# Kernel tuning notes

Hardware: AMD Instinct MI355X
Metric: run time of the kernel (lower is better)

## Reference

```python
import jax, jax.numpy as jnp
import numpy as np

C_IN = 4
C_OUT = 8
K = 5            # kernel_size (hardcoded by reshape(25,2) in original)
N_ROT = 8
R_B = 8          # rot_basis_size
STRIDE = 1
PAD = 2
TWO_PI = 2.0 * np.pi
ROT_SCALE = TWO_PI / R_B


def B2(x):
    # quadratic B-spline, exactly as in the torch source
    return (-3 * (-0.5 + x) ** 2 * jnp.sign(0.5 - x)
            + (-1.5 + x) ** 2 * jnp.sign(1.5 - x)
            - 3 * (1 + 2 * x) ** 2 * jnp.sign(0.5 + x) / 4
            + (3 + 2 * x) ** 2 * jnp.sign(1.5 + x) / 4) / 4


def angle_dist(th1, th2):
    return jnp.mod(th2 - th1 + np.pi, TWO_PI) - np.pi


def make_kernel_stack(weights):
    # weights: (C_IN, R_B*K*K, C_OUT). M = K*K*R_B combined (spatial-center, rot-center) index;
    # original repeats each spatial center R_B times (np.repeat) and tiles rot centers K*K times.
    lidx = -(K // 2)
    coords = jnp.arange(lidx, K // 2 + 1, dtype=jnp.float32)
    grid = jnp.stack(jnp.meshgrid(coords, coords, indexing='ij'), axis=-1)  # (K,K,2), grid[i,j]=[i+l, j+l]
    centers_xy = jnp.repeat(grid.reshape(K * K, 2), R_B, axis=0)            # (M,2)
    rot_centers = jnp.tile(jnp.arange(R_B, dtype=jnp.float32) * ROT_SCALE, K * K)  # (M,)
    rot_sample = jnp.arange(N_ROT, dtype=jnp.float32) * (TWO_PI / N_ROT)    # (N_ROT,)

    def one_kernel(theta):
        c, s = jnp.cos(theta), jnp.sin(theta)
        x, y = grid[..., 0], grid[..., 1]
        xxs = jnp.stack([x * c - y * s, x * s + y * c], axis=-1)            # (K,K,2) rotated sample grid
        xx_diffs = centers_xy[None, None, :, :] - xxs[:, :, None, :]        # (K,K,M,2)
        xx_vals = jnp.prod(B2(xx_diffs), axis=-1)                           # (K,K,M) separable spatial spline
        rots = rot_sample + theta                                           # (N_ROT,)
        rot_vals = B2(angle_dist(rots[:, None], rot_centers[None, :]) / ROT_SCALE)  # (N_ROT,M)
        vals = xx_vals[:, :, None, :] * rot_vals[None, None, :, :]          # (K,K,N_ROT,M)
        # contract basis index m against weights -> (C_OUT, C_IN, N_ROT, K, K)
        return jnp.einsum('xyrm,imo->oirxy', vals, weights)

    ks = jax.vmap(one_kernel)(-rot_sample)  # (N_ROT, C_OUT, C_IN, N_ROT, K, K), matches torch.cat over -theta
    return ks.reshape(N_ROT * C_OUT, C_IN * N_ROT, K, K)


def setup_inputs() -> dict:
    key = jax.random.key(0)
    kx, kw = jax.random.split(key)
    X = jax.random.normal(kx, (8, C_IN, N_ROT, 256, 256), dtype=jnp.float32)
    weights = jax.random.normal(kw, (C_IN, R_B * K * K, C_OUT), dtype=jnp.float32)
    return {'X': X, 'weights': weights}


def reference(X, weights):
    ks = make_kernel_stack(weights)                       # (N_ROT*C_OUT, C_IN*N_ROT, K, K)
    B, c, d, H, W = X.shape
    Xr = X.reshape(B, c * d, H, W)
    out = jax.lax.conv_general_dilated(
        Xr, ks, window_strides=(STRIDE, STRIDE),
        padding=[(PAD, PAD), (PAD, PAD)],
        dimension_numbers=('NCHW', 'OIHW', 'NCHW'))        # (B, N_ROT*C_OUT, h, w)
    Bn, _, h, w = out.shape
    out = out.reshape(Bn, N_ROT, C_OUT, h, w).transpose(0, 2, 1, 3, 4)  # (B, C_OUT, N_ROT, h, w)
    return (TWO_PI / N_ROT) * out
```

## Files before the change

kernel.cpp:

```cpp
#include <hip/hip_runtime.h>
#include <hip/hip_fp16.h>
#include <math.h>

#define PI_F      3.14159265358979323846f
#define TWO_PI_F  6.28318530717958647692f
#define PI4_F     0.78539816339744830962f

typedef _Float16 f16x8 __attribute__((ext_vector_type(8)));
typedef float    f32x4 __attribute__((ext_vector_type(4)));

#define XH_OFF     ((size_t)1 << 20)
#define XH_BYTES   ((size_t)8 * 256 * 256 * 32 * 2)

__device__ __forceinline__ float sgn(float t) {
    return (t > 0.f) ? 1.f : ((t < 0.f) ? -1.f : 0.f);
}

__device__ __forceinline__ float b2(float x) {
    float a = x - 0.5f;
    float b = x - 1.5f;
    float c = 1.f + 2.f * x;
    float d = 3.f + 2.f * x;
    return (-3.f * a * a * sgn(0.5f - x)
            + b * b * sgn(1.5f - x)
            - 0.75f * c * c * sgn(0.5f + x)
            + 0.25f * d * d * sgn(1.5f + x)) * 0.25f;
}

__global__ void build_ks_kernel(const float* __restrict__ w, __half* __restrict__ ksh) {
    int g = blockIdx.x * 256 + threadIdx.x;
    if (g >= 64 * 32 * 25) return;
    int O = g & 63;
    int rest = g >> 6;
    int t = rest % 25;
    int I = rest / 25;
    int r0 = O >> 3, o = O & 7;
    int i = I >> 3, r = I & 7;
    int x = t / 5, y = t % 5;

    float theta = -(float)r0 * PI4_F;
    float cth = cosf(theta), sth = sinf(theta);
    float fx = (float)(x - 2), fy = (float)(y - 2);
    float xc = fx * cth - fy * sth;
    float yc = fx * sth + fy * cth;

    float rotv[8];
    float rs = (float)r * PI4_F + theta;
    #pragma unroll
    for (int mr = 0; mr < 8; ++mr) {
        float v = (float)mr * PI4_F - rs + PI_F;
        float md = fmodf(v, TWO_PI_F);
        if (md < 0.f) md += TWO_PI_F;
        rotv[mr] = b2((md - PI_F) / PI4_F);
    }

    float sum = 0.f;
    for (int mx = 0; mx < 25; ++mx) {
        float cx = (float)(mx / 5 - 2);
        float cy = (float)(mx % 5 - 2);
        float bx = b2(cx - xc) * b2(cy - yc);
        if (bx != 0.f) {
            const float* wp = w + (size_t)(i * 200 + mx * 8) * 8 + o;
            #pragma unroll
            for (int mr = 0; mr < 8; ++mr)
                sum = fmaf(bx * rotv[mr], wp[mr * 8], sum);
        }
    }
    ksh[(size_t)(t * 64 + O) * 32 + I] = __float2half(sum);
}

__global__ __launch_bounds__(256, 4) void hwc_kernel(const float* __restrict__ X,
                                                     __half* __restrict__ Xh) {
    int b = blockIdx.x >> 8;
    int h = blockIdx.x & 255;
    int ww = threadIdx.x;
    const float* Xb = X + ((size_t)b * 32) * 65536 + h * 256 + ww;

    union { __half hh[8]; uint4 u; } pk[4];
    #pragma unroll
    for (int c = 0; c < 32; ++c)
        pk[c >> 3].hh[c & 7] = __float2half(Xb[(size_t)c * 65536]);

    uint4* dst = (uint4*)(Xh + ((size_t)(b * 65536 + h * 256 + ww)) * 32);
    #pragma unroll
    for (int kk = 0; kk < 4; ++kk) dst[kk] = pk[kk].u;
}

__global__ __launch_bounds__(512, 2) void conv_hwc_kernel(const __half* __restrict__ Xh,
                                                          const __half* __restrict__ ksh,
                                                          float* __restrict__ out) {
    __shared__ uint4 xt[4 * 1297];

    int bid = blockIdx.x;
    int b   = bid >> 6;
    int rem = bid & 63;
    int h0  = (rem >> 3) << 5;
    int w0  = (rem & 7) << 5;
    int tid = threadIdx.x;

    const char* Xb = (const char*)Xh + (size_t)b * ((size_t)65536 * 64);

    for (int p = tid; p < 1296; p += 512) {
        int r = p / 36, c = p - (p / 36) * 36;
        int gh = h0 + r - 2;
        int gw = w0 + c - 2;
        uint4 v0 = make_uint4(0u, 0u, 0u, 0u), v1 = v0, v2 = v0, v3 = v0;
        if ((unsigned)gh < 256u && (unsigned)gw < 256u) {
            const uint4* s = (const uint4*)(Xb + ((size_t)(gh * 256 + gw)) * 64);
            v0 = s[0]; v1 = s[1]; v2 = s[2]; v3 = s[3];
        }
        xt[0 * 1297 + p] = v0;
        xt[1 * 1297 + p] = v1;
        xt[2 * 1297 + p] = v2;
        xt[3 * 1297 + p] = v3;
    }
    __syncthreads();

    int wave = tid >> 6, lane = tid & 63;
    int lO = lane & 15, ks4 = lane >> 4;
    int bidx = lO * 4 + ks4;
    const uint4* ksq = (const uint4*)ksh;

    f32x4 acc[8][4] = {};
    int baseA[8];
    #pragma unroll
    for (int m = 0; m < 8; ++m)
        baseA[m] = 1297 * ks4 + (wave * 4 + (m >> 1)) * 36 + (m & 1) * 16 + lO;

    f16x8 Bf[2][4];
    #pragma unroll
    for (int n = 0; n < 4; ++n)
        Bf[0][n] = __builtin_bit_cast(f16x8, ksq[n * 64 + bidx]);

    #pragma unroll
    for (int t = 0; t < 25; ++t) {
        const int cur = t & 1, nxt = cur ^ 1;

        if (t < 24) {
            const int t1 = t + 1;
            #pragma unroll
            for (int n = 0; n < 4; ++n)
                Bf[nxt][n] = __builtin_bit_cast(f16x8, ksq[t1 * 256 + n * 64 + bidx]);
        }

        const int aoff = (t / 5) * 36 + (t % 5);
        f16x8 Af[8];
        #pragma unroll
        for (int m = 0; m < 8; ++m)
            Af[m] = __builtin_bit_cast(f16x8, xt[baseA[m] + aoff]);

        #pragma unroll
        for (int m = 0; m < 8; ++m) {
            #pragma unroll
            for (int n = 0; n < 4; ++n)
                acc[m][n] = __builtin_amdgcn_mfma_f32_16x16x32_f16(Af[m], Bf[cur][n], acc[m][n], 0, 0, 0);
        }

        if ((t & 1) == 1 && t < 24) __syncthreads();
    }

    #pragma unroll
    for (int m = 0; m < 8; ++m) {
        int gh  = h0 + wave * 4 + (m >> 1);
        int gwb = w0 + (m & 1) * 16 + ks4 * 4;
        #pragma unroll
        for (int n = 0; n < 4; ++n) {
            int O = n * 16 + lO;
            float* op = out + (((size_t)(b * 8 + (O & 7)) * 8 + (O >> 3)) << 16)
                            + gh * 256 + gwb;
            *(f32x4*)op = acc[m][n] * PI4_F;
        }
    }
}

__global__ __launch_bounds__(512, 4) void conv_kernel_f32(const float* __restrict__ X,
                                                          const __half* __restrict__ ksh,
                                                          float* __restrict__ out) {
    __shared__ uint4 xt[720 * 5];
    int blk = blockIdx.x;
    int b = blk >> 7;
    int rem = blk & 127;
    int h0 = (rem >> 3) << 4;
    int w0 = (rem & 7) << 5;
    int tid = threadIdx.x;
    const float* Xb = X + (size_t)b * 32 * 65536;
    for (int lin = tid; lin < 2880; lin += 512) {
        int slotq = lin / 720;
        int pxi = lin - slotq * 720;
        int r = pxi / 36;
        int c = pxi - r * 36;
        int gh = h0 + r - 2;
        int gw = w0 + c - 2;
        union { __half h[8]; uint4 u; } pk;
        if ((unsigned)gh < 256u && (unsigned)gw < 256u) {
            const float* src = Xb + (size_t)slotq * 8 * 65536 + gh * 256 + gw;
            #pragma unroll
            for (int j = 0; j < 8; ++j) pk.h[j] = __float2half(src[j * 65536]);
        } else {
            pk.u = make_uint4(0u, 0u, 0u, 0u);
        }
        xt[pxi * 5 + slotq] = pk.u;
    }
    __syncthreads();
    int wave = tid >> 6, lane = tid & 63;
    int lO = lane & 15, ks4 = lane >> 4;
    const uint4* ksq = (const uint4*)ksh;
    int bidx = lO * 4 + ks4;
    f32x4 acc[4][4] = {};
    int baseA[4];
    #pragma unroll
    for (int q = 0; q < 4; ++q)
        baseA[q] = ((wave * 2 + (q >> 1)) * 36 + (q & 1) * 16 + lO) * 5 + ks4;
    f16x8 Bf[2][4];
    #pragma unroll
    for (int n = 0; n < 4; ++n)
        Bf[0][n] = __builtin_bit_cast(f16x8, ksq[n * 64 + bidx]);
    #pragma unroll
    for (int t = 0; t < 25; ++t) {
        const int cur = t & 1, nxt = cur ^ 1;
        f16x8 Af[4];
        #pragma unroll
        for (int q = 0; q < 4; ++q)
            Af[q] = __builtin_bit_cast(f16x8, xt[baseA[q] + ((t / 5) * 36 + (t % 5)) * 5]);
        if (t < 24) {
            #pragma unroll
            for (int n = 0; n < 4; ++n)
                Bf[nxt][n] = __builtin_bit_cast(f16x8, ksq[(t + 1) * 256 + n * 64 + bidx]);
        }
        #pragma unroll
        for (int q = 0; q < 4; ++q)
            #pragma unroll
            for (int n = 0; n < 4; ++n)
                acc[q][n] = __builtin_amdgcn_mfma_f32_16x16x32_f16(Af[q], Bf[cur][n], acc[q][n], 0, 0, 0);
    }
    #pragma unroll
    for (int q = 0; q < 4; ++q) {
        int gh = h0 + wave * 2 + (q >> 1);
        int gwb = w0 + (q & 1) * 16 + ks4 * 4;
        #pragma unroll
        for (int n = 0; n < 4; ++n) {
            int O = n * 16 + lO;
            float* op = out + (((size_t)(b * 8 + (O & 7)) * 8 + (O >> 3)) << 16) + gh * 256 + gwb;
            *(f32x4*)op = acc[q][n] * PI4_F;
        }
    }
}

extern "C" void kernel_launch(void* const* d_in, const int* in_sizes, int n_in,
                              void* d_out, int out_size, void* d_ws, size_t ws_size,
                              hipStream_t stream) {
    const float* X = (const float*)d_in[0];
    const float* w = (const float*)d_in[1];
    float* outp = (float*)d_out;
    char* ws = (char*)d_ws;
    __half* ksh = (__half*)ws;

    build_ks_kernel<<<200, 256, 0, stream>>>(w, ksh);

    if (ws_size >= XH_OFF + XH_BYTES) {
        __half* Xh = (__half*)(ws + XH_OFF);
        hwc_kernel<<<8 * 256, 256, 0, stream>>>(X, Xh);
        conv_hwc_kernel<<<8 * 64, 512, 0, stream>>>(Xh, ksh, outp);
    } else {
        conv_kernel_f32<<<8 * 16 * 8, 512, 0, stream>>>(X, ksh, outp);
    }
}
```

Measured before the change: 105.2 us.

## Stage conv weights in LDS in two halves and double-buffer A/B fragments

Measured after the change: 110.5 us. +5.1%, slower.

```diff
diff --git a/kernel.cpp b/kernel.cpp
--- a/kernel.cpp
+++ b/kernel.cpp
@@ -90,6 +90,7 @@
                                                           const __half* __restrict__ ksh,
                                                           float* __restrict__ out) {
     __shared__ uint4 xt[4 * 1297];
+    __shared__ uint4 ks_s[13 * 256];
 
     int bid = blockIdx.x;
     int b   = bid >> 6;
@@ -99,6 +100,7 @@
     int tid = threadIdx.x;
 
     const char* Xb = (const char*)Xh + (size_t)b * ((size_t)65536 * 64);
+    const uint4* ksq = (const uint4*)ksh;
 
     for (int p = tid; p < 1296; p += 512) {
         int r = p / 36, c = p - (p / 36) * 36;
@@ -114,12 +116,16 @@
         xt[2 * 1297 + p] = v2;
         xt[3 * 1297 + p] = v3;
     }
+    #pragma unroll
+    for (int k = 0; k < 7; ++k) {
+        int lin = tid + k * 512;
+        if (lin < 3328) ks_s[lin] = ksq[lin];
+    }
     __syncthreads();
 
     int wave = tid >> 6, lane = tid & 63;
     int lO = lane & 15, ks4 = lane >> 4;
     int bidx = lO * 4 + ks4;
-    const uint4* ksq = (const uint4*)ksh;
 
     f32x4 acc[8][4] = {};
     int baseA[8];
@@ -127,36 +133,72 @@
     for (int m = 0; m < 8; ++m)
         baseA[m] = 1297 * ks4 + (wave * 4 + (m >> 1)) * 36 + (m & 1) * 16 + lO;
 
-    f16x8 Bf[2][4];
+    f16x8 Af[2][8], Bf[2][4];
+
+    #pragma unroll
+    for (int m = 0; m < 8; ++m)
+        Af[0][m] = __builtin_bit_cast(f16x8, xt[baseA[m]]);
     #pragma unroll
     for (int n = 0; n < 4; ++n)
-        Bf[0][n] = __builtin_bit_cast(f16x8, ksq[n * 64 + bidx]);
-
-    #pragma unroll
-    for (int t = 0; t < 25; ++t) {
+        Bf[0][n] = __builtin_bit_cast(f16x8, ks_s[n * 64 + bidx]);
+
+    #pragma unroll
+    for (int t = 0; t < 13; ++t) {
         const int cur = t & 1, nxt = cur ^ 1;
-
+        if (t < 12) {
+            const int t1 = t + 1;
+            const int aoff = (t1 / 5) * 36 + (t1 % 5);
+            #pragma unroll
+            for (int m = 0; m < 8; ++m)
+                Af[nxt][m] = __builtin_bit_cast(f16x8, xt[baseA[m] + aoff]);
+            #pragma unroll
+            for (int n = 0; n < 4; ++n)
+                Bf[nxt][n] = __builtin_bit_cast(f16x8, ks_s[t1 * 256 + n * 64 + bidx]);
+        }
+        #pragma unroll
+        for (int m = 0; m < 8; ++m) {
+            #pragma unroll
+            for (int n = 0; n < 4; ++n)
+                acc[m][n] = __builtin_amdgcn_mfma_f32_16x16x32_f16(Af[cur][m], Bf[cur][n], acc[m][n], 0, 0, 0);
+        }
+    }
+
+    __syncthreads();
+    #pragma unroll
+    for (int k = 0; k < 6; ++k) {
+        int lin = tid + k * 512;
+        if (lin < 3072) ks_s[lin] = ksq[3328 + lin];
+    }
+    __syncthreads();
+
+    {
+        const int aoff13 = (13 / 5) * 36 + (13 % 5);
+        #pragma unroll
+        for (int m = 0; m < 8; ++m)
+            Af[1][m] = __builtin_bit_cast(f16x8, xt[baseA[m] + aoff13]);
+        #pragma unroll
+        for (int n = 0; n < 4; ++n)
+            Bf[1][n] = __builtin_bit_cast(f16x8, ks_s[n * 64 + bidx]);
+    }
+    #pragma unroll
+    for (int t = 13; t < 25; ++t) {
+        const int cur = t & 1, nxt = cur ^ 1;
         if (t < 24) {
             const int t1 = t + 1;
-            #pragma unroll
-            for (int n = 0; n < 4; ++n)
-                Bf[nxt][n] = __builtin_bit_cast(f16x8, ksq[t1 * 256 + n * 64 + bidx]);
-        }
-
-        const int aoff = (t / 5) * 36 + (t % 5);
-        f16x8 Af[8];
-        #pragma unroll
-        for (int m = 0; m < 8; ++m)
-            Af[m] = __builtin_bit_cast(f16x8, xt[baseA[m] + aoff]);
-
+            const int aoff = (t1 / 5) * 36 + (t1 % 5);
+            #pragma unroll
+            for (int m = 0; m < 8; ++m)
+                Af[nxt][m] = __builtin_bit_cast(f16x8, xt[baseA[m] + aoff]);
+            #pragma unroll
+            for (int n = 0; n < 4; ++n)
+                Bf[nxt][n] = __builtin_bit_cast(f16x8, ks_s[(t1 - 13) * 256 + n * 64 + bidx]);
+        }
         #pragma unroll
         for (int m = 0; m < 8; ++m) {
             #pragma unroll
             for (int n = 0; n < 4; ++n)
-                acc[m][n] = __builtin_amdgcn_mfma_f32_16x16x32_f16(Af[m], Bf[cur][n], acc[m][n], 0, 0, 0);
-        }
-
-        if ((t & 1) == 1 && t < 24) __syncthreads();
+                acc[m][n] = __builtin_amdgcn_mfma_f32_16x16x32_f16(Af[cur][m], Bf[cur][n], acc[m][n], 0, 0, 0);
+        }
     }
 
     #pragma unroll
```
